# Kernel tuning notes

Measured on AMD Instinct MI355X. Metric: run time of the kernel, lower is better.

Reference implementation:

```python
import jax, jax.numpy as jnp
import numpy as np

M0, M1 = 16, 8          # scalar / vector multiplicities (16x0e + 8x1o)
NB = 16                  # number_of_basis
RMAX = 8.0               # max_radius
N_NODES, N_EDGES = 10000, 160000
WNUM = M0*M0 + M0*M1 + M1*M1 + M1*M0  # 576, tp weight_numel


def sus(t):
    """e3nn soft_unit_step: exp(-1/t) for t>0 else 0."""
    safe = jnp.where(t > 0, t, 1.0)
    return jnp.where(t > 0, jnp.exp(-1.0 / safe), 0.0)


def setup_inputs():
    key = jax.random.key(0)
    ks = jax.random.split(key, 12)
    D = M0 + 3 * M1  # 40
    x = jax.random.normal(ks[0], (N_NODES, D), jnp.float32)
    edge_index = jax.random.randint(ks[1], (2, N_EDGES), 0, N_NODES, jnp.int32)
    edge_attr = jax.random.normal(ks[2], (N_EDGES, 4), jnp.float32)  # sh lmax=1
    node_attr = jnp.ones((N_NODES, 1), jnp.float32)
    batch = jnp.zeros((N_NODES,), jnp.int32)
    amf = jax.random.uniform(ks[3], (N_EDGES, 1), jnp.float32) * RMAX  # edge lengths
    Wq0 = jax.random.normal(ks[4], (M0, M0), jnp.float32)
    Wq1 = jax.random.normal(ks[5], (M1, M1), jnp.float32)
    Wk1 = jax.random.normal(ks[6], (NB, 16), jnp.float32)
    Wk2 = jax.random.normal(ks[7], (16, WNUM), jnp.float32)
    Wv1 = jax.random.normal(ks[8], (NB, 16), jnp.float32)
    Wv2 = jax.random.normal(ks[9], (16, WNUM), jnp.float32)
    Wd0 = jax.random.normal(ks[10], (M0, M0), jnp.float32)
    Wd1 = jax.random.normal(ks[11], (M1, M1), jnp.float32)
    return dict(x=x, edge_index=edge_index, edge_attr=edge_attr, node_attr=node_attr,
                batch=batch, additional_message_features=amf,
                Wq0=Wq0, Wq1=Wq1, Wk1=Wk1, Wk2=Wk2, Wv1=Wv1, Wv2=Wv2, Wd0=Wd0, Wd1=Wd1)


def reference(x, edge_index, edge_attr, node_attr, batch, additional_message_features,
              Wq0, Wq1, Wk1, Wk2, Wv1, Wv2, Wd0, Wd1):
    n = x.shape[0]
    src, dst = edge_index[0], edge_index[1]
    d = additional_message_features.reshape(-1)  # [E]

    # soft_one_hot_linspace(basis='smooth_finite', cutoff=True) * sqrt(NB)
    centers = jnp.linspace(0.0, RMAX, NB + 2)[1:-1]
    step = RMAX / (NB + 1)
    diff = (d[:, None] - centers) / step
    emb = (1.14136 * np.exp(2.0)) * sus(diff + 1.0) * sus(1.0 - diff) * np.sqrt(NB)  # [E,NB]
    cutoff = sus(10.0 * (1.0 - d / RMAX))  # [E]

    # split irreps: scalars [*,M0], vectors [*,M1,3]
    x0 = x[:, :M0]
    x1 = x[:, M0:].reshape(n, M1, 3)

    # q = Linear(input_irreps -> hidden_irreps): per-irrep linear, 1/sqrt(fan_in)
    q0 = (x0 @ Wq0) / np.sqrt(M0)
    q1 = jnp.einsum('nui,uw->nwi', x1, Wq1) / np.sqrt(M1)

    # radial MLPs producing per-edge tensor-product weights
    def radial(W1, W2):
        h = jax.nn.silu((emb @ W1) / np.sqrt(NB))
        return (h @ W2) / np.sqrt(16.0)  # [E, WNUM]
    wk = radial(Wk1, Wk2)
    wv = radial(Wv1, Wv2)

    xs0, xs1 = x0[src], x1[src]           # gather by edge source
    sh0, sh1 = edge_attr[:, 0], edge_attr[:, 1:4]
    dot11 = jnp.einsum('eui,ei->eu', xs1, sh1) / np.sqrt(3.0)  # 1o x 1o -> 0e CG

    def fctp(w):
        # FullyConnectedTensorProduct(input, sh, out) with per-edge weights.
        s1 = M0 * M0
        s2 = s1 + M0 * M1
        s3 = s2 + M1 * M1
        w1 = w[:, :s1].reshape(-1, M0, M0)   # 0e x 0e -> 0e
        w2 = w[:, s1:s2].reshape(-1, M0, M1) # 0e x 1o -> 1o
        w3 = w[:, s2:s3].reshape(-1, M1, M1) # 1o x 0e -> 1o
        w4 = w[:, s3:].reshape(-1, M1, M0)   # 1o x 1o -> 0e
        norm = 1.0 / np.sqrt(M0 + M1)        # path fan-in normalization
        o0 = (jnp.einsum('euw,eu->ew', w1, xs0 * sh0[:, None]) +
              jnp.einsum('euw,eu->ew', w4, dot11)) * norm            # [E,M0]
        o1 = (jnp.einsum('euw,eu,ei->ewi', w2, xs0, sh1) +
              jnp.einsum('euw,eui->ewi', w3, xs1 * sh0[:, None, None])) * norm  # [E,M1,3]
        return o0, o1

    k0, k1 = fctp(wk)
    v0, v1 = fctp(wv)

    # dot: FullyConnectedTensorProduct(hidden, hidden, '0e') with shared weights
    score = (jnp.einsum('eu,ev,uv->e', q0[dst], k0, Wd0) +
             jnp.einsum('eui,evi,uv->e', q1[dst], k1, Wd1) / np.sqrt(3.0)) / np.sqrt(M0*M0 + M1*M1)

    expv = cutoff * jnp.exp(score)                                   # [E]
    z = jax.ops.segment_sum(expv, dst, num_segments=n)               # [N]
    z = jnp.where(z == 0, 1.0, z)
    alpha = expv / z[dst]
    we = jnp.sqrt(jax.nn.relu(alpha))                                # alpha.relu().sqrt()
    v = jnp.concatenate([v0, v1.reshape(-1, 3 * M1)], axis=1)        # [E,40]
    return jax.ops.segment_sum(we[:, None] * v, dst, num_segments=n) # [N,40]
```

## Files before the change

kernel.cpp:

```cpp
#include <hip/hip_runtime.h>
#include <hip/hip_bf16.h>

#define E_CNT 160000
#define N_CNT 10000

#define INV_STEP   2.125f
#define EMB_C      33.734292f
#define INVS320    0.05590170f
#define INVS8      0.35355339f
#define INV_SQRT3  0.57735027f
#define KSCALE     0.051031036f

#define OFF_FLAG   0
#define OFF_EAF    400016
#define OFF_AMFF   1040016
#define OFF_WK1F   1200656
#define OFF_WV1F   1200912
#define OFF_P      1219600
#define OFF_EXPV   1619600
#define OFF_VBUF   1779600
#define OFF_DEG    8179600
#define OFF_Z      8179600
#define OFF_DEG2   8189600
#define OFF_START  8199600
#define OFF_START2 8209601
#define OFF_CURS   8219602
#define OFF_CURS2  8229602
#define OFF_DPOS   8239602
#define OFF_ELIST2 8399602
#define OFF_G      8559632

static __device__ __forceinline__ float bf2f(__hip_bfloat16 b) { return __bfloat162float(b); }
static __device__ __forceinline__ float cvt(float v) { return v; }
static __device__ __forceinline__ float cvt(__hip_bfloat16 v) { return bf2f(v); }
static __device__ __forceinline__ float sanitize(float v) {
    return fminf(fmaxf(v, -1e30f), 1e30f);
}
static __device__ __forceinline__ unsigned short f2bf(float f) {
    unsigned x = __float_as_uint(f);
    unsigned r = (x + 0x7fffu + ((x >> 16) & 1u)) >> 16;
    return (unsigned short)r;
}
static __device__ __forceinline__ float bflo(unsigned u) { return __uint_as_float(u << 16); }
static __device__ __forceinline__ float bfhi(unsigned u) { return __uint_as_float(u & 0xffff0000u); }

static __device__ __forceinline__ float4 load4(const void* p, int i4, int f32)
{
    if (f32) return ((const float4*)p)[i4];
    uint2 u = ((const uint2*)p)[i4];
    float4 r;
    r.x = bflo(u.x); r.y = bfhi(u.x);
    r.z = bflo(u.y); r.w = bfhi(u.y);
    return r;
}

static __device__ __forceinline__ void ld8(const float* p, float (&r)[8])
{
    float4 a = ((const float4*)p)[0];
    float4 b = ((const float4*)p)[1];
    r[0] = a.x; r[1] = a.y; r[2] = a.z; r[3] = a.w;
    r[4] = b.x; r[5] = b.y; r[6] = b.z; r[7] = b.w;
}
static __device__ __forceinline__ void ld8(const __hip_bfloat16* p, float (&r)[8])
{
    uint4 u = *(const uint4*)p;
    r[0] = bflo(u.x); r[1] = bfhi(u.x); r[2] = bflo(u.y); r[3] = bfhi(u.y);
    r[4] = bflo(u.z); r[5] = bfhi(u.z); r[6] = bflo(u.w); r[7] = bfhi(u.w);
}

template <typename T>
static __device__ __forceinline__ void build_G(
    const T* __restrict__ x, const T* __restrict__ W2b, int n, int p, int c, float* __restrict__ ws)
{
    float xs[40];
#pragma unroll
    for (int q = 0; q < 5; ++q) ld8(x + n * 40 + q * 8, *(float(*)[8])(xs + q * 8));
    const T* W2 = W2b + c * 576;

    float out[96];
#pragma unroll
    for (int k = 0; k < 96; ++k) out[k] = 0.f;

#pragma unroll
    for (int u = 0; u < 16; ++u) {
        float r0[8], r1[8];
        ld8(W2 + u * 16, r0);
        ld8(W2 + u * 16 + 8, r1);
        const float xv = xs[u];
#pragma unroll
        for (int w = 0; w < 8; ++w) {
            out[w]     = fmaf(r0[w], xv, out[w]);
            out[8 + w] = fmaf(r1[w], xv, out[8 + w]);
        }
    }
#pragma unroll
    for (int u = 0; u < 16; ++u) {
        float r[8];
        ld8(W2 + 256 + u * 8, r);
        const float xv = xs[u];
#pragma unroll
        for (int w = 0; w < 8; ++w) out[16 + w] = fmaf(r[w], xv, out[16 + w]);
    }
#pragma unroll
    for (int u = 0; u < 8; ++u) {
        float r[8];
        ld8(W2 + 384 + u * 8, r);
        const float a0 = xs[16 + u * 3 + 0];
        const float a1 = xs[16 + u * 3 + 1];
        const float a2 = xs[16 + u * 3 + 2];
#pragma unroll
        for (int w = 0; w < 8; ++w) {
            out[24 + w * 3 + 0] = fmaf(r[w], a0, out[24 + w * 3 + 0]);
            out[24 + w * 3 + 1] = fmaf(r[w], a1, out[24 + w * 3 + 1]);
            out[24 + w * 3 + 2] = fmaf(r[w], a2, out[24 + w * 3 + 2]);
        }
    }
#pragma unroll
    for (int u = 0; u < 8; ++u) {
        float r0[8], r1[8];
        ld8(W2 + 448 + u * 16, r0);
        ld8(W2 + 448 + u * 16 + 8, r1);
        const float a0 = xs[16 + u * 3 + 0];
        const float a1 = xs[16 + u * 3 + 1];
        const float a2 = xs[16 + u * 3 + 2];
#pragma unroll
        for (int w = 0; w < 8; ++w) {
            out[48 + w * 3 + 0] = fmaf(r0[w], a0, out[48 + w * 3 + 0]);
            out[48 + w * 3 + 1] = fmaf(r0[w], a1, out[48 + w * 3 + 1]);
            out[48 + w * 3 + 2] = fmaf(r0[w], a2, out[48 + w * 3 + 2]);
            out[48 + (8 + w) * 3 + 0] = fmaf(r1[w], a0, out[48 + (8 + w) * 3 + 0]);
            out[48 + (8 + w) * 3 + 1] = fmaf(r1[w], a1, out[48 + (8 + w) * 3 + 1]);
            out[48 + (8 + w) * 3 + 2] = fmaf(r1[w], a2, out[48 + (8 + w) * 3 + 2]);
        }
    }
#pragma unroll
    for (int k = 0; k < 48; ++k) out[48 + k] *= INV_SQRT3;

    uint4 ov[12];
    unsigned* ou = (unsigned*)ov;
#pragma unroll
    for (int k = 0; k < 48; ++k)
        ou[k] = (unsigned)f2bf(out[2 * k]) | ((unsigned)f2bf(out[2 * k + 1]) << 16);
    uint4* dp = (uint4*)((unsigned short*)(ws + OFF_G) + ((size_t)n * 2 + p) * 1536 + c * 96);
#pragma unroll
    for (int q = 0; q < 12; ++q) dp[q] = ov[q];
}

template <typename T>
static __device__ __forceinline__ void build_P(
    const T* __restrict__ x, const T* __restrict__ Wq0, const T* __restrict__ Wq1,
    const T* __restrict__ Wd0, const T* __restrict__ Wd1, int n, float* __restrict__ ws)
{
    float xs[40];
#pragma unroll
    for (int q = 0; q < 5; ++q) ld8(x + n * 40 + q * 8, *(float(*)[8])(xs + q * 8));

    float q0[16];
#pragma unroll
    for (int w = 0; w < 16; ++w) q0[w] = 0.f;
#pragma unroll
    for (int u = 0; u < 16; ++u) {
        float r0[8], r1[8];
        ld8(Wq0 + u * 16, r0);
        ld8(Wq0 + u * 16 + 8, r1);
        const float xv = xs[u];
#pragma unroll
        for (int w = 0; w < 8; ++w) {
            q0[w]     = fmaf(r0[w], xv, q0[w]);
            q0[8 + w] = fmaf(r1[w], xv, q0[8 + w]);
        }
    }
#pragma unroll
    for (int w = 0; w < 16; ++w) q0[w] *= 0.25f;

    float p0[16];
#pragma unroll
    for (int v = 0; v < 16; ++v) p0[v] = 0.f;
#pragma unroll
    for (int w = 0; w < 16; ++w) {
        float r0[8], r1[8];
        ld8(Wd0 + w * 16, r0);
        ld8(Wd0 + w * 16 + 8, r1);
        const float qv = q0[w];
#pragma unroll
        for (int v = 0; v < 8; ++v) {
            p0[v]     = fmaf(r0[v], qv, p0[v]);
            p0[8 + v] = fmaf(r1[v], qv, p0[8 + v]);
        }
    }
    float* pn = ws + OFF_P + n * 40;
#pragma unroll
    for (int v = 0; v < 16; ++v) pn[v] = sanitize(p0[v] * INVS320);

    float q1[24];
#pragma unroll
    for (int k = 0; k < 24; ++k) q1[k] = 0.f;
#pragma unroll
    for (int u = 0; u < 8; ++u) {
        float r[8];
        ld8(Wq1 + u * 8, r);
        const float a0 = xs[16 + u * 3 + 0];
        const float a1 = xs[16 + u * 3 + 1];
        const float a2 = xs[16 + u * 3 + 2];
#pragma unroll
        for (int w = 0; w < 8; ++w) {
            q1[w * 3 + 0] = fmaf(r[w], a0, q1[w * 3 + 0]);
            q1[w * 3 + 1] = fmaf(r[w], a1, q1[w * 3 + 1]);
            q1[w * 3 + 2] = fmaf(r[w], a2, q1[w * 3 + 2]);
        }
    }
#pragma unroll
    for (int k = 0; k < 24; ++k) q1[k] *= INVS8;

    float p1[24];
#pragma unroll
    for (int k = 0; k < 24; ++k) p1[k] = 0.f;
#pragma unroll
    for (int w = 0; w < 8; ++w) {
        float r[8];
        ld8(Wd1 + w * 8, r);
        const float b0 = q1[w * 3 + 0];
        const float b1 = q1[w * 3 + 1];
        const float b2 = q1[w * 3 + 2];
#pragma unroll
        for (int v = 0; v < 8; ++v) {
            p1[v * 3 + 0] = fmaf(r[v], b0, p1[v * 3 + 0]);
            p1[v * 3 + 1] = fmaf(r[v], b1, p1[v * 3 + 1]);
            p1[v * 3 + 2] = fmaf(r[v], b2, p1[v * 3 + 2]);
        }
    }
    const float sc = INVS320 * INV_SQRT3;
#pragma unroll
    for (int k = 0; k < 24; ++k) pn[16 + k] = sanitize(p1[k] * sc);
}

__global__ __launch_bounds__(256) void prepgp_kernel(
    const void* __restrict__ x,   const void* __restrict__ ea,  const void* __restrict__ amf,
    const void* __restrict__ Wq0, const void* __restrict__ Wq1,
    const void* __restrict__ Wk1, const void* __restrict__ Wk2,
    const void* __restrict__ Wv1, const void* __restrict__ Wv2,
    const void* __restrict__ Wd0, const void* __restrict__ Wd1,
    const int* __restrict__ ei, float* __restrict__ ws)
{
    __shared__ int sflag;
    const int tid = threadIdx.x;
    const int blk = blockIdx.x;
    if (tid == 0) {
        const unsigned short* xb = (const unsigned short*)x;
        int cnt = 0;
        for (int k = 0; k < 256; k += 2) {
            unsigned e = (unsigned)((xb[k] >> 7) & 0xFF);
            if (e >= 141) ++cnt;
        }
        sflag = (cnt >= 8) ? 1 : 0;
        if (blk == 0) *(int*)ws = sflag;
    }
    __syncthreads();
    const int f32 = sflag;

    if (blk < 625) {
        const int i = blk * 256 + tid;
        if (i < 160000) ((float4*)(ws + OFF_EAF))[i] = load4(ea, i, f32);
        if (i < 40000) {
            ((float4*)(ws + OFF_AMFF))[i] = load4(amf, i, f32);
#pragma unroll
            for (int k = 0; k < 4; ++k) {
                atomicAdd((int*)(ws + OFF_DEG)  + ei[E_CNT + 4 * i + k], 1);
                atomicAdd((int*)(ws + OFF_DEG2) + ei[4 * i + k], 1);
            }
        }
        if (i < 64) {
            ((float4*)(ws + OFF_WK1F))[i] = load4(Wk1, i, f32);
            ((float4*)(ws + OFF_WV1F))[i] = load4(Wv1, i, f32);
        }
        return;
    }
    if (blk < 1875) {
        const int t = (blk - 625) * 256 + tid;
        const int p   = t / 160000;
        const int rem = t - p * 160000;
        const int c   = rem / 10000;
        const int n   = rem - c * 10000;
        const void* W2b = p ? Wv2 : Wk2;
        if (f32) build_G((const float*)x, (const float*)W2b, n, p, c, ws);
        else     build_G((const __hip_bfloat16*)x, (const __hip_bfloat16*)W2b, n, p, c, ws);
        return;
    }
    {
        const int n = (blk - 1875) * 256 + tid;
        if (n >= N_CNT) return;
        if (f32) build_P((const float*)x, (const float*)Wq0, (const float*)Wq1,
                         (const float*)Wd0, (const float*)Wd1, n, ws);
        else     build_P((const __hip_bfloat16*)x, (const __hip_bfloat16*)Wq0,
                         (const __hip_bfloat16*)Wq1, (const __hip_bfloat16*)Wd0,
                         (const __hip_bfloat16*)Wd1, n, ws);
    }
}

__global__ __launch_bounds__(512) void scan_kernel(float* __restrict__ ws)
{
    __shared__ int ssum[512];
    const int t    = threadIdx.x;
    const int half = t >> 8;
    const int lt   = t & 255;
    int* deg   = (int*)(ws + (half ? OFF_DEG2   : OFF_DEG));
    int* start = (int*)(ws + (half ? OFF_START2 : OFF_START));
    int* curs  = (int*)(ws + (half ? OFF_CURS2  : OFF_CURS));
    const int base = lt * 40;
    int s = 0;
    for (int k = 0; k < 40; ++k) {
        int idx = base + k;
        if (idx < N_CNT) s += deg[idx];
    }
    ssum[t] = s;
    __syncthreads();
    for (int off = 1; off < 256; off <<= 1) {
        int v = (lt >= off) ? ssum[t - off] : 0;
        __syncthreads();
        ssum[t] += v;
        __syncthreads();
    }
    int run = ssum[t] - s;
    for (int k = 0; k < 40; ++k) {
        int idx = base + k;
        if (idx < N_CNT) {
            start[idx] = run;
            curs[idx]  = run;
            run += deg[idx];
        }
    }
    if (lt == 255) start[N_CNT] = E_CNT;
    __syncthreads();
    for (int k = t; k < N_CNT; k += 512) ws[OFF_Z + k] = 0.f;
}

__global__ __launch_bounds__(256) void fill_kernel(const int* __restrict__ ei, float* __restrict__ ws)
{
    const int e = blockIdx.x * 256 + threadIdx.x;
    int pd = atomicAdd((int*)(ws + OFF_CURS)  + ei[E_CNT + e], 1);
    int ps = atomicAdd((int*)(ws + OFF_CURS2) + ei[e], 1);
    ((int*)(ws + OFF_ELIST2))[ps] = e;
    ((int*)(ws + OFF_DPOS))[ps]   = pd;
}

static __device__ __forceinline__ void load48(unsigned (&ub)[48], const uint4* __restrict__ rp)
{
#pragma unroll
    for (int q = 0; q < 12; ++q) {
        uint4 v = rp[q];
        ub[4 * q + 0] = v.x; ub[4 * q + 1] = v.y;
        ub[4 * q + 2] = v.z; ub[4 * q + 3] = v.w;
    }
}

static __device__ __forceinline__ void accum48(const unsigned (&ub)[48], float hc, float sh0,
    float s1x, float s1y, float s1z,
    float (&o0)[16], float (&o1)[24], float (&t2a)[8])
{
    const float hs = hc * sh0;
#define GVAL(k) (((k) & 1) ? bfhi(ub[(k) >> 1]) : bflo(ub[(k) >> 1]))
#pragma unroll
    for (int w = 0; w < 16; ++w) o0[w] = fmaf(hs, GVAL(w), o0[w]);
#pragma unroll
    for (int w = 0; w < 8; ++w) t2a[w] = fmaf(hc, GVAL(16 + w), t2a[w]);
#pragma unroll
    for (int k = 0; k < 24; ++k) o1[k] = fmaf(hs, GVAL(24 + k), o1[k]);
#pragma unroll
    for (int w = 0; w < 16; ++w) {
        float g = GVAL(48 + w * 3 + 0) * s1x;
        g = fmaf(GVAL(48 + w * 3 + 1), s1y, g);
        g = fmaf(GVAL(48 + w * 3 + 2), s1z, g);
        o0[w] = fmaf(hc, g, o0[w]);
    }
#undef GVAL
}

__global__ __launch_bounds__(128, 2) void edge_kernel(
    const int* __restrict__ ei, float* __restrict__ ws)
{
    const int tid  = threadIdx.x;
    const int pass = tid >> 6;
    const int lane = tid & 63;
    const int b  = blockIdx.x;
    const int lb = (b < 2496) ? ((b & 7) * 312 + (b >> 3)) : b;
    const int sidx = lb * 64 + lane;
    const int e    = ((const int*)(ws + OFF_ELIST2))[sidx];
    const int dpos = ((const int*)(ws + OFF_DPOS))[sidx];
    const int src  = ei[e];
    const int dst  = ei[E_CNT + e];

    const uint4* Gp = (const uint4*)((const unsigned short*)(ws + OFF_G)
                                     + ((size_t)src * 2 + pass) * 1536);
    unsigned A[48], B[48];
    load48(A, Gp);
    load48(B, Gp + 12);

    const float d   = ws[OFF_AMFF + e];
    const float dsv = d * INV_STEP;
    float emb[16];
#pragma unroll
    for (int bb = 0; bb < 16; ++bb) {
        float t1 = dsv - (float)bb;
        float t2 = (float)(bb + 2) - dsv;
        float v = 0.f;
        if (t1 > 0.f && t2 > 0.f) v = EMB_C * expf(-1.f / t1 - 1.f / t2);
        emb[bb] = v;
    }

    const float* W1 = ws + (pass ? OFF_WV1F : OFF_WK1F);
    float h[16];
#pragma unroll
    for (int j = 0; j < 16; ++j) {
        float s = 0.f;
#pragma unroll
        for (int bb = 0; bb < 16; ++bb) s = fmaf(emb[bb], W1[bb * 16 + j], s);
        s *= 0.25f;
        h[j] = s / (1.f + expf(-s));
    }

    const float4 eav = ((const float4*)(ws + OFF_EAF))[e];
    const float sh0 = eav.x, s1x = eav.y, s1y = eav.z, s1z = eav.w;

    float o0[16], o1[24], t2a[8];
#pragma unroll
    for (int i = 0; i < 16; ++i) o0[i] = 0.f;
#pragma unroll
    for (int i = 0; i < 24; ++i) o1[i] = 0.f;
#pragma unroll
    for (int i = 0; i < 8; ++i) t2a[i] = 0.f;

#pragma unroll
    for (int c = 0; c < 16; c += 2) {
        accum48(A, h[c], sh0, s1x, s1y, s1z, o0, o1, t2a);
        if (c + 2 < 16) load48(A, Gp + (c + 2) * 12);
        accum48(B, h[c + 1], sh0, s1x, s1y, s1z, o0, o1, t2a);
        if (c + 3 < 16) load48(B, Gp + (c + 3) * 12);
    }

#pragma unroll
    for (int w = 0; w < 8; ++w) {
        o1[w * 3 + 0] = fmaf(t2a[w], s1x, o1[w * 3 + 0]);
        o1[w * 3 + 1] = fmaf(t2a[w], s1y, o1[w * 3 + 1]);
        o1[w * 3 + 2] = fmaf(t2a[w], s1z, o1[w * 3 + 2]);
    }

    if (pass == 0) {
        const float* pd = ws + OFF_P + dst * 40;
        float sc = 0.f;
#pragma unroll
        for (int j = 0; j < 16; ++j) sc = fmaf(o0[j], pd[j], sc);
#pragma unroll
        for (int j = 0; j < 24; ++j) sc = fmaf(o1[j], pd[16 + j], sc);
        sc = fminf(fmaxf(sc * KSCALE, -60.f), 60.f);
        float ct = 10.f * (1.f - d * 0.125f);
        float cutoff = (ct > 0.f) ? expf(-1.f / ct) : 0.f;
        float ev = fmaxf(cutoff * expf(sc), 0.f);
        ws[OFF_EXPV + dpos] = ev;
        atomicAdd(ws + OFF_Z + dst, ev);
    } else {
        float* vr = ws + OFF_VBUF + (size_t)dpos * 40;
#pragma unroll
        for (int j = 0; j < 16; ++j) vr[j] = sanitize(o0[j] * KSCALE);
#pragma unroll
        for (int j = 0; j < 24; ++j) vr[16 + j] = sanitize(o1[j] * KSCALE);
    }
}

__global__ __launch_bounds__(256) void gather_kernel(
    const float* __restrict__ ws, void* __restrict__ out)
{
    const int i = blockIdx.x * 256 + threadIdx.x;
    if (i >= N_CNT * 10) return;
    const int n = i / 10;
    const int q = i - n * 10;
    const int* start = (const int*)(ws + OFF_START);
    const float* expv = ws + OFF_EXPV;
    const float4* Vbuf4 = (const float4*)(ws + OFF_VBUF);
    const int s = start[n], t = start[n + 1];

    float zz = ws[OFF_Z + n];
    const float rz = (zz > 0.f) ? 1.f / zz : 1.f;

    float ax = 0.f, ay = 0.f, az = 0.f, aw = 0.f;
    for (int j = s; j < t; ++j) {
        const float we = sqrtf(fmaxf(expv[j] * rz, 0.f));
        float4 v = Vbuf4[(size_t)j * 10 + q];
        ax = fmaf(we, v.x, ax); ay = fmaf(we, v.y, ay);
        az = fmaf(we, v.z, az); aw = fmaf(we, v.w, aw);
    }
    ax = sanitize(ax); ay = sanitize(ay); az = sanitize(az); aw = sanitize(aw);
    const int f32 = *(const int*)ws;
    if (f32) {
        float4 o; o.x = ax; o.y = ay; o.z = az; o.w = aw;
        ((float4*)out)[(size_t)n * 10 + q] = o;
    } else {
        uint2 o;
        o.x = (unsigned)f2bf(ax) | ((unsigned)f2bf(ay) << 16);
        o.y = (unsigned)f2bf(az) | ((unsigned)f2bf(aw) << 16);
        ((uint2*)out)[(size_t)n * 10 + q] = o;
    }
}

extern "C" void kernel_launch(void* const* d_in, const int* in_sizes, int n_in,
                              void* d_out, int out_size, void* d_ws, size_t ws_size,
                              hipStream_t stream)
{
    (void)in_sizes; (void)n_in; (void)out_size; (void)ws_size;
    const void* x   = d_in[0];
    const int*  ei  = (const int*)d_in[1];
    const void* ea  = d_in[2];
    const void* amf = d_in[5];
    const void* Wq0 = d_in[6];
    const void* Wq1 = d_in[7];
    const void* Wk1 = d_in[8];
    const void* Wk2 = d_in[9];
    const void* Wv1 = d_in[10];
    const void* Wv2 = d_in[11];
    const void* Wd0 = d_in[12];
    const void* Wd1 = d_in[13];

    float* ws = (float*)d_ws;

    hipMemsetAsync(ws + OFF_DEG, 0, 20000 * sizeof(int), stream);
    prepgp_kernel<<<1915, 256, 0, stream>>>(x, ea, amf, Wq0, Wq1, Wk1, Wk2, Wv1, Wv2, Wd0, Wd1, ei, ws);
    scan_kernel<<<1, 512, 0, stream>>>(ws);
    fill_kernel<<<625, 256, 0, stream>>>(ei, ws);
    edge_kernel<<<2500, 128, 0, stream>>>(ei, ws);
    gather_kernel<<<(N_CNT * 10 + 255) / 256, 256, 0, stream>>>(ws, d_out);
}
```

Before: 301.4 us.

## Transpose G table to structure-of-arrays and split prep kernel into detect/prep/gp

Changes the per-node precomputed G table from one contiguous 3 KB row per node and pass to a layout of 16-byte chunks strided by node. Each G write in the build kernel and each gather in the edge kernel now touches a separate plane. The fused prep kernel is split into a single-wave dtype detect kernel, an edge-data prep kernel, and a G/P build kernel, so the per-block serial detect loop is gone. Stores from the build kernel become coalesced across nodes. Edge-kernel loads, which are indexed by random src, now hit 12 separate 16-byte lines per chunk instead of contiguous 192-byte spans, which may hurt gather locality.

```diff
diff --git a/kernel.cpp b/kernel.cpp
--- a/kernel.cpp
+++ b/kernel.cpp
@@ -30,6 +30,7 @@
 #define OFF_ELIST2 8399602
 #define OFF_G      8559632
 
+
 static __device__ __forceinline__ float bf2f(__hip_bfloat16 b) { return __bfloat162float(b); }
 static __device__ __forceinline__ float cvt(float v) { return v; }
 static __device__ __forceinline__ float cvt(__hip_bfloat16 v) { return bf2f(v); }
@@ -66,6 +67,39 @@
     uint4 u = *(const uint4*)p;
     r[0] = bflo(u.x); r[1] = bfhi(u.x); r[2] = bflo(u.y); r[3] = bfhi(u.y);
     r[4] = bflo(u.z); r[5] = bfhi(u.z); r[6] = bflo(u.w); r[7] = bfhi(u.w);
+}
+
+__global__ void detect_kernel(const unsigned short* __restrict__ xb, int* __restrict__ flag)
+{
+    const int lane = threadIdx.x;
+    unsigned e0 = (unsigned)((xb[2 * lane] >> 7) & 0xFF);
+    unsigned e1 = (unsigned)((xb[128 + 2 * lane] >> 7) & 0xFF);
+    int c = (e0 >= 141 ? 1 : 0) + (e1 >= 141 ? 1 : 0);
+#pragma unroll
+    for (int off = 1; off < 64; off <<= 1) c += __shfl_xor(c, off);
+    if (lane == 0) *flag = (c >= 8) ? 1 : 0;
+}
+
+__global__ __launch_bounds__(256) void prep_kernel(
+    const void* __restrict__ ea, const void* __restrict__ amf,
+    const void* __restrict__ Wk1, const void* __restrict__ Wv1,
+    const int* __restrict__ ei, float* __restrict__ ws)
+{
+    const int f32 = *(const int*)ws;
+    const int i = blockIdx.x * 256 + threadIdx.x;
+    if (i < 160000) ((float4*)(ws + OFF_EAF))[i] = load4(ea, i, f32);
+    if (i < 40000) {
+        ((float4*)(ws + OFF_AMFF))[i] = load4(amf, i, f32);
+#pragma unroll
+        for (int k = 0; k < 4; ++k) {
+            atomicAdd((int*)(ws + OFF_DEG)  + ei[E_CNT + 4 * i + k], 1);
+            atomicAdd((int*)(ws + OFF_DEG2) + ei[4 * i + k], 1);
+        }
+    }
+    if (i < 64) {
+        ((float4*)(ws + OFF_WK1F))[i] = load4(Wk1, i, f32);
+        ((float4*)(ws + OFF_WV1F))[i] = load4(Wv1, i, f32);
+    }
 }
 
 template <typename T>
@@ -141,9 +175,9 @@
 #pragma unroll
     for (int k = 0; k < 48; ++k)
         ou[k] = (unsigned)f2bf(out[2 * k]) | ((unsigned)f2bf(out[2 * k + 1]) << 16);
-    uint4* dp = (uint4*)((unsigned short*)(ws + OFF_G) + ((size_t)n * 2 + p) * 1536 + c * 96);
-#pragma unroll
-    for (int q = 0; q < 12; ++q) dp[q] = ov[q];
+    uint4* gb = (uint4*)(ws + OFF_G) + (size_t)(p * 16 + c) * 120000 + n;
+#pragma unroll
+    for (int q = 0; q < 12; ++q) gb[q * 10000] = ov[q];
 }
 
 template <typename T>
@@ -234,49 +268,18 @@
     for (int k = 0; k < 24; ++k) pn[16 + k] = sanitize(p1[k] * sc);
 }
 
-__global__ __launch_bounds__(256) void prepgp_kernel(
-    const void* __restrict__ x,   const void* __restrict__ ea,  const void* __restrict__ amf,
+__global__ __launch_bounds__(256) void gp_kernel(
+    const void* __restrict__ x,
     const void* __restrict__ Wq0, const void* __restrict__ Wq1,
-    const void* __restrict__ Wk1, const void* __restrict__ Wk2,
-    const void* __restrict__ Wv1, const void* __restrict__ Wv2,
+    const void* __restrict__ Wk2, const void* __restrict__ Wv2,
     const void* __restrict__ Wd0, const void* __restrict__ Wd1,
-    const int* __restrict__ ei, float* __restrict__ ws)
-{
-    __shared__ int sflag;
+    float* __restrict__ ws)
+{
+    const int f32 = *(const int*)ws;
     const int tid = threadIdx.x;
     const int blk = blockIdx.x;
-    if (tid == 0) {
-        const unsigned short* xb = (const unsigned short*)x;
-        int cnt = 0;
-        for (int k = 0; k < 256; k += 2) {
-            unsigned e = (unsigned)((xb[k] >> 7) & 0xFF);
-            if (e >= 141) ++cnt;
-        }
-        sflag = (cnt >= 8) ? 1 : 0;
-        if (blk == 0) *(int*)ws = sflag;
-    }
-    __syncthreads();
-    const int f32 = sflag;
-
-    if (blk < 625) {
-        const int i = blk * 256 + tid;
-        if (i < 160000) ((float4*)(ws + OFF_EAF))[i] = load4(ea, i, f32);
-        if (i < 40000) {
-            ((float4*)(ws + OFF_AMFF))[i] = load4(amf, i, f32);
-#pragma unroll
-            for (int k = 0; k < 4; ++k) {
-                atomicAdd((int*)(ws + OFF_DEG)  + ei[E_CNT + 4 * i + k], 1);
-                atomicAdd((int*)(ws + OFF_DEG2) + ei[4 * i + k], 1);
-            }
-        }
-        if (i < 64) {
-            ((float4*)(ws + OFF_WK1F))[i] = load4(Wk1, i, f32);
-            ((float4*)(ws + OFF_WV1F))[i] = load4(Wv1, i, f32);
-        }
-        return;
-    }
-    if (blk < 1875) {
-        const int t = (blk - 625) * 256 + tid;
+    if (blk < 1250) {
+        const int t = blk * 256 + tid;
         const int p   = t / 160000;
         const int rem = t - p * 160000;
         const int c   = rem / 10000;
@@ -287,7 +290,7 @@
         return;
     }
     {
-        const int n = (blk - 1875) * 256 + tid;
+        const int n = (blk - 1250) * 256 + tid;
         if (n >= N_CNT) return;
         if (f32) build_P((const float*)x, (const float*)Wq0, (const float*)Wq1,
                          (const float*)Wd0, (const float*)Wd1, n, ws);
@@ -343,11 +346,11 @@
     ((int*)(ws + OFF_DPOS))[ps]   = pd;
 }
 
-static __device__ __forceinline__ void load48(unsigned (&ub)[48], const uint4* __restrict__ rp)
+static __device__ __forceinline__ void load48p(unsigned (&ub)[48], const uint4* __restrict__ p0)
 {
 #pragma unroll
     for (int q = 0; q < 12; ++q) {
-        uint4 v = rp[q];
+        uint4 v = p0[(size_t)q * 10000];
         ub[4 * q + 0] = v.x; ub[4 * q + 1] = v.y;
         ub[4 * q + 2] = v.z; ub[4 * q + 3] = v.w;
     }
@@ -389,11 +392,10 @@
     const int src  = ei[e];
     const int dst  = ei[E_CNT + e];
 
-    const uint4* Gp = (const uint4*)((const unsigned short*)(ws + OFF_G)
-                                     + ((size_t)src * 2 + pass) * 1536);
+    const uint4* gb = (const uint4*)(ws + OFF_G) + (size_t)pass * 1920000 + src;
     unsigned A[48], B[48];
-    load48(A, Gp);
-    load48(B, Gp + 12);
+    load48p(A, gb);
+    load48p(B, gb + 120000);
 
     const float d   = ws[OFF_AMFF + e];
     const float dsv = d * INV_STEP;
@@ -432,9 +434,9 @@
 #pragma unroll
     for (int c = 0; c < 16; c += 2) {
         accum48(A, h[c], sh0, s1x, s1y, s1z, o0, o1, t2a);
-        if (c + 2 < 16) load48(A, Gp + (c + 2) * 12);
+        if (c + 2 < 16) load48p(A, gb + (size_t)(c + 2) * 120000);
         accum48(B, h[c + 1], sh0, s1x, s1y, s1z, o0, o1, t2a);
-        if (c + 3 < 16) load48(B, Gp + (c + 3) * 12);
+        if (c + 3 < 16) load48p(B, gb + (size_t)(c + 3) * 120000);
     }
 
 #pragma unroll
@@ -522,7 +524,9 @@
     float* ws = (float*)d_ws;
 
     hipMemsetAsync(ws + OFF_DEG, 0, 20000 * sizeof(int), stream);
-    prepgp_kernel<<<1915, 256, 0, stream>>>(x, ea, amf, Wq0, Wq1, Wk1, Wk2, Wv1, Wv2, Wd0, Wd1, ei, ws);
+    detect_kernel<<<1, 64, 0, stream>>>((const unsigned short*)x, (int*)ws);
+    prep_kernel<<<625, 256, 0, stream>>>(ea, amf, Wk1, Wv1, ei, ws);
+    gp_kernel<<<1290, 256, 0, stream>>>(x, Wq0, Wq1, Wk2, Wv2, Wd0, Wd1, ws);
     scan_kernel<<<1, 512, 0, stream>>>(ws);
     fill_kernel<<<625, 256, 0, stream>>>(ei, ws);
     edge_kernel<<<2500, 128, 0, stream>>>(ei, ws);
```

After: 283.9 us. 5.8% less time.
